# Performance work log

Hardware: AMD Instinct MI355X
Metric: run time of the kernel (lower is better)

## Reference

```python
import jax, jax.numpy as jnp
import numpy as np

B, S, H, E, TOP_K = 4, 2048, 1024, 16, 4


def setup_inputs() -> dict:
    key = jax.random.key(0)
    ks = jax.random.split(key, 12)
    sc = 1.0 / np.sqrt(H)
    inp = {
        "x": jax.random.normal(ks[0], (B, S, H), dtype=jnp.float32),
        "image": jax.random.normal(ks[1], (B, S, H), dtype=jnp.float32),
        "text": jax.random.normal(ks[2], (B, S, H), dtype=jnp.float32),
        "audio": jax.random.normal(ks[3], (B, S, H), dtype=jnp.float32),
        # generalized router linear
        "Wg": jax.random.uniform(ks[4], (H, E), jnp.float32, -sc, sc),
        "bg": jax.random.uniform(ks[5], (E,), jnp.float32, -sc, sc),
        # per-modality router linears
        "Wi": jax.random.uniform(ks[6], (H, E), jnp.float32, -sc, sc),
        "bi": jax.random.uniform(ks[7], (E,), jnp.float32, -sc, sc),
        "Wt": jax.random.uniform(ks[8], (H, E), jnp.float32, -sc, sc),
        "bt": jax.random.uniform(ks[9], (E,), jnp.float32, -sc, sc),
        "Wa": jax.random.uniform(ks[10], (H, E), jnp.float32, -sc, sc),
        "ba": jax.random.uniform(ks[11], (E,), jnp.float32, -sc, sc),
    }
    return inp


def reference(x, image, text, audio, Wg, bg, Wi, bi, Wt, bt, Wa, ba):
    # combined_logits = generalized_router(x) + sum_m modality_router_m(modality_m)
    logits = (
        jnp.einsum("bsh,he->bse", x, Wg) + bg
        + jnp.einsum("bsh,he->bse", image, Wi) + bi
        + jnp.einsum("bsh,he->bse", text, Wt) + bt
        + jnp.einsum("bsh,he->bse", audio, Wa) + ba
    )  # [B,S,E]
    router_probs = jax.nn.softmax(logits, axis=-1)
    top_k_probs, top_k_indices = jax.lax.top_k(router_probs, TOP_K)
    top_k_probs = top_k_probs / jnp.sum(top_k_probs, axis=-1, keepdims=True)
    prob_per_expert = jnp.mean(router_probs, axis=(0, 1))  # [E]
    aux_loss = jnp.sum(prob_per_expert * jnp.log(prob_per_expert * E + 1e-9))
    return (top_k_indices, top_k_probs, aux_loss)
```

## Files before the change

### kernel.cpp

```cpp
#include <hip/hip_runtime.h>
#include <math.h>

constexpr int kTokens = 8192;
constexpr int kH      = 1024;
constexpr int kE      = 16;
constexpr int kTopK   = 4;

template<int NC>
__global__ __launch_bounds__(256, 4)
void router_fmac(const float* __restrict__ x,   const float* __restrict__ img,
                 const float* __restrict__ txt, const float* __restrict__ aud,
                 const float* __restrict__ Wg,  const float* __restrict__ Wi,
                 const float* __restrict__ Wt,  const float* __restrict__ Wa,
                 float* __restrict__ partials)
{
    constexpr int KEXT = 4096 / NC;
    constexpr int P    = KEXT / 16;
    constexpr int MS   = NC / 4;

    __shared__ float xt[2][256 * 20];

    const int t   = threadIdx.x;
    const int w   = t >> 6;
    const int ln  = t & 63;
    const int tq  = ln >> 2;
    const int eq  = ln & 3;
    const int bid = blockIdx.x;
    const int ks  = bid & (NC - 1);
    const int tg  = bid / NC;
    const int m   = ks / MS;
    const int h0  = (ks % MS) * KEXT;
    const int tok0 = tg * 256;

    const float* Xm = (m == 0) ? x  : (m == 1) ? img : (m == 2) ? txt : aud;
    const float* Wm = (m == 0) ? Wg : (m == 1) ? Wi  : (m == 2) ? Wt  : Wa;

    const int sc = t & 3;
    const int sr = t >> 2;
    const float* gbase = Xm + (size_t)tok0 * kH + h0 + sc * 4;

    float4 pf[4];

#pragma unroll
    for (int i = 0; i < 4; ++i)
        pf[i] = *(const float4*)(gbase + (size_t)(sr + 64 * i) * kH);
#pragma unroll
    for (int i = 0; i < 4; ++i)
        *(float4*)&xt[0][(sr + 64 * i) * 20 + sc * 4] = pf[i];
    __syncthreads();

    float facc[4][4];
#pragma unroll
    for (int i = 0; i < 4; ++i)
#pragma unroll
        for (int q = 0; q < 4; ++q) facc[i][q] = 0.f;

    const int r0 = w * 64 + tq;

#pragma unroll
    for (int p = 0; p < P; ++p) {
        if (p < P - 1) {
#pragma unroll
            for (int i = 0; i < 4; ++i)
                pf[i] = *(const float4*)(gbase + (size_t)(sr + 64 * i) * kH + (p + 1) * 16);
        }

        const float* buf = xt[p & 1];
        const float* wp  = Wm + (size_t)(h0 + p * 16) * kE + eq * 4;

#pragma unroll
        for (int hg = 0; hg < 4; ++hg) {
            float4 wv[4];
#pragma unroll
            for (int j = 0; j < 4; ++j)
                wv[j] = *(const float4*)(wp + (hg * 4 + j) * kE);
            float4 xv[4];
#pragma unroll
            for (int i = 0; i < 4; ++i)
                xv[i] = *(const float4*)&buf[(r0 + 16 * i) * 20 + hg * 4];
#pragma unroll
            for (int j = 0; j < 4; ++j) {
#pragma unroll
                for (int i = 0; i < 4; ++i) {
                    const float xh = (j == 0) ? xv[i].x : (j == 1) ? xv[i].y
                                   : (j == 2) ? xv[i].z : xv[i].w;
                    facc[i][0] += xh * wv[j].x;  facc[i][1] += xh * wv[j].y;
                    facc[i][2] += xh * wv[j].z;  facc[i][3] += xh * wv[j].w;
                }
            }
        }

        if (p < P - 1) {
#pragma unroll
            for (int i = 0; i < 4; ++i)
                *(float4*)&xt[(p + 1) & 1][(sr + 64 * i) * 20 + sc * 4] = pf[i];
        }
        __syncthreads();
    }

#pragma unroll
    for (int i = 0; i < 4; ++i) {
        const int token = tok0 + w * 64 + tq + 16 * i;
        *(float4*)&partials[((size_t)ks * kTokens + token) * kE + eq * 4] =
            make_float4(facc[i][0], facc[i][1], facc[i][2], facc[i][3]);
    }
}

template<int NC>
__global__ __launch_bounds__(256)
void router_topk(const float* __restrict__ partials,
                 const float* __restrict__ bg, const float* __restrict__ bi,
                 const float* __restrict__ bt, const float* __restrict__ ba,
                 float* __restrict__ out, float* __restrict__ blocksum)
{
    __shared__ double lgs[64][kE + 1];
    __shared__ float  pr[64][kE + 1];

    const int t    = threadIdx.x;
    const int tq   = t >> 2;
    const int eq   = t & 3;
    const int tok0 = blockIdx.x * 64;

    double a0 = (double)bg[eq*4+0] + (double)bi[eq*4+0] + (double)bt[eq*4+0] + (double)ba[eq*4+0];
    double a1 = (double)bg[eq*4+1] + (double)bi[eq*4+1] + (double)bt[eq*4+1] + (double)ba[eq*4+1];
    double a2 = (double)bg[eq*4+2] + (double)bi[eq*4+2] + (double)bt[eq*4+2] + (double)ba[eq*4+2];
    double a3 = (double)bg[eq*4+3] + (double)bi[eq*4+3] + (double)bt[eq*4+3] + (double)ba[eq*4+3];

#pragma unroll
    for (int c = 0; c < NC; ++c) {
        const float4 v = *(const float4*)(partials + ((size_t)c * kTokens + tok0 + tq) * kE + eq * 4);
        a0 += (double)v.x;  a1 += (double)v.y;  a2 += (double)v.z;  a3 += (double)v.w;
    }
    lgs[tq][eq*4+0] = a0;  lgs[tq][eq*4+1] = a1;
    lgs[tq][eq*4+2] = a2;  lgs[tq][eq*4+3] = a3;
    __syncthreads();

    if (t < 64) {
        const int tok = tok0 + t;
        double lg[kE];
#pragma unroll
        for (int e = 0; e < kE; ++e) lg[e] = lgs[t][e];

        double mx = lg[0];
#pragma unroll
        for (int e = 1; e < kE; ++e) mx = fmax(mx, lg[e]);

        float p[kE];
        float sum = 0.f;
#pragma unroll
        for (int e = 0; e < kE; ++e) {
            p[e] = expf((float)(lg[e] - mx));
            sum += p[e];
        }
        const float inv = 1.f / sum;
#pragma unroll
        for (int e = 0; e < kE; ++e) { p[e] *= inv; pr[t][e] = p[e]; }

        unsigned used = 0;
        float tp[kTopK];
        int   ti[kTopK];
        float s4 = 0.f;
#pragma unroll
        for (int k = 0; k < kTopK; ++k) {
            float best = -1.f;
            int   bidx = 0;
#pragma unroll
            for (int e = 0; e < kE; ++e) {
                if (!((used >> e) & 1u) && p[e] > best) { best = p[e]; bidx = e; }
            }
            used |= 1u << bidx;
            tp[k] = best;
            ti[k] = bidx;
            s4 += best;
        }
        const float rn = 1.f / s4;

        *(float4*)&out[(size_t)tok * kTopK] =
            make_float4((float)ti[0], (float)ti[1], (float)ti[2], (float)ti[3]);
        *(float4*)&out[(size_t)kTokens * kTopK + (size_t)tok * kTopK] =
            make_float4(tp[0] * rn, tp[1] * rn, tp[2] * rn, tp[3] * rn);
    }
    __syncthreads();

    if (t < kE) {
        float s = 0.f;
#pragma unroll
        for (int tk = 0; tk < 64; ++tk) s += pr[tk][t];
        blocksum[blockIdx.x * kE + t] = s;
    }
}

__global__ __launch_bounds__(64)
void router_aux(const float* __restrict__ blocksum, float* __restrict__ out)
{
    __shared__ double ps[kE];
    const int t = threadIdx.x;
    if (t < kE) {
        double s = 0.0;
        for (int b = 0; b < 128; ++b) s += (double)blocksum[b * kE + t];
        ps[t] = s / (double)kTokens;
    }
    __syncthreads();
    if (t == 0) {
        double aux = 0.0;
#pragma unroll
        for (int e = 0; e < kE; ++e) aux += ps[e] * log(ps[e] * (double)kE + 1e-9);
        out[(size_t)kTokens * kTopK * 2] = (float)aux;
    }
}

extern "C" void kernel_launch(void* const* d_in, const int* in_sizes, int n_in,
                              void* d_out, int out_size, void* d_ws, size_t ws_size,
                              hipStream_t stream)
{
    const float* x   = (const float*)d_in[0];
    const float* img = (const float*)d_in[1];
    const float* txt = (const float*)d_in[2];
    const float* aud = (const float*)d_in[3];
    const float* Wg  = (const float*)d_in[4];
    const float* bg  = (const float*)d_in[5];
    const float* Wi  = (const float*)d_in[6];
    const float* bi  = (const float*)d_in[7];
    const float* Wt  = (const float*)d_in[8];
    const float* bt  = (const float*)d_in[9];
    const float* Wa  = (const float*)d_in[10];
    const float* ba  = (const float*)d_in[11];

    float* out = (float*)d_out;

    const size_t need32 = (size_t)32 * kTokens * kE * 4 + 128 * kE * 4;
    if (ws_size >= need32) {
        float* partials = (float*)d_ws;
        float* blocksum = (float*)((char*)d_ws + (size_t)32 * kTokens * kE * 4);
        router_fmac<32><<<1024, 256, 0, stream>>>(x, img, txt, aud, Wg, Wi, Wt, Wa, partials);
        router_topk<32><<<128, 256, 0, stream>>>(partials, bg, bi, bt, ba, out, blocksum);
        router_aux<<<1, 64, 0, stream>>>(blocksum, out);
    } else {
        float* partials = (float*)d_ws;
        float* blocksum = (float*)((char*)d_ws + (size_t)16 * kTokens * kE * 4);
        router_fmac<16><<<512, 256, 0, stream>>>(x, img, txt, aud, Wg, Wi, Wt, Wa, partials);
        router_topk<16><<<128, 256, 0, stream>>>(partials, bg, bi, bt, ba, out, blocksum);
        router_aux<<<1, 64, 0, stream>>>(blocksum, out);
    }
}
```

Before: 211.7 us.

## Drop LDS staging in router matmul; use single-wave blocks with lane-split H and shuffle reduce

The router GEMV kernel no longer stages X tiles through double-buffered shared memory with block barriers. Each 64-lane block now covers 64 tokens, and each lane reads float4 slices of H directly from global memory while computing all 16 experts. A two-step xor-shuffle then reduces across the 4 lanes that share a token. This removes the LDS traffic and __syncthreads, but raises register pressure (64 accumulators per lane) and gives strided, less coalesced global loads.

```diff
diff --git a/kernel.cpp b/kernel.cpp
--- a/kernel.cpp
+++ b/kernel.cpp
@@ -7,7 +7,7 @@
 constexpr int kTopK   = 4;
 
 template<int NC>
-__global__ __launch_bounds__(256, 4)
+__global__ __launch_bounds__(64, 4)
 void router_fmac(const float* __restrict__ x,   const float* __restrict__ img,
                  const float* __restrict__ txt, const float* __restrict__ aud,
                  const float* __restrict__ Wg,  const float* __restrict__ Wi,
@@ -15,94 +15,83 @@
                  float* __restrict__ partials)
 {
     constexpr int KEXT = 4096 / NC;
-    constexpr int P    = KEXT / 16;
+    constexpr int NQ   = KEXT / 16;
     constexpr int MS   = NC / 4;
 
-    __shared__ float xt[2][256 * 20];
-
-    const int t   = threadIdx.x;
-    const int w   = t >> 6;
-    const int ln  = t & 63;
-    const int tq  = ln >> 2;
-    const int eq  = ln & 3;
-    const int bid = blockIdx.x;
-    const int ks  = bid & (NC - 1);
-    const int tg  = bid / NC;
-    const int m   = ks / MS;
-    const int h0  = (ks % MS) * KEXT;
-    const int tok0 = tg * 256;
+    const int ln = threadIdx.x;
+    const int tq = ln >> 2;
+    const int eq = ln & 3;
+    const int ks = blockIdx.x >> 7;
+    const int tg = blockIdx.x & 127;
+    const int m  = ks / MS;
+    const int h0 = (ks % MS) * KEXT;
+    const int tok0 = tg * 64;
 
     const float* Xm = (m == 0) ? x  : (m == 1) ? img : (m == 2) ? txt : aud;
     const float* Wm = (m == 0) ? Wg : (m == 1) ? Wi  : (m == 2) ? Wt  : Wa;
 
-    const int sc = t & 3;
-    const int sr = t >> 2;
-    const float* gbase = Xm + (size_t)tok0 * kH + h0 + sc * 4;
-
-    float4 pf[4];
-
+    float facc[4][kE];
 #pragma unroll
     for (int i = 0; i < 4; ++i)
-        pf[i] = *(const float4*)(gbase + (size_t)(sr + 64 * i) * kH);
+#pragma unroll
+        for (int e = 0; e < kE; ++e) facc[i][e] = 0.f;
+
+    const float* xp[4];
 #pragma unroll
     for (int i = 0; i < 4; ++i)
-        *(float4*)&xt[0][(sr + 64 * i) * 20 + sc * 4] = pf[i];
-    __syncthreads();
-
-    float facc[4][4];
+        xp[i] = Xm + (size_t)(tok0 + tq + 16 * i) * kH + h0 + eq * 4;
+    const float* wp = Wm + (size_t)(h0 + eq * 4) * kE;
+
+#pragma unroll 2
+    for (int q = 0; q < NQ; ++q) {
+        float4 xv[4];
+#pragma unroll
+        for (int i = 0; i < 4; ++i)
+            xv[i] = *(const float4*)(xp[i] + q * 16);
+
+#pragma unroll
+        for (int j = 0; j < 4; ++j) {
+            const float* wr = wp + (size_t)(q * 16 + j) * kE;
+            const float4 w0 = ((const float4*)wr)[0];
+            const float4 w1 = ((const float4*)wr)[1];
+            const float4 w2 = ((const float4*)wr)[2];
+            const float4 w3 = ((const float4*)wr)[3];
+#pragma unroll
+            for (int i = 0; i < 4; ++i) {
+                const float xh = (j == 0) ? xv[i].x : (j == 1) ? xv[i].y
+                               : (j == 2) ? xv[i].z : xv[i].w;
+                facc[i][0]  += xh * w0.x;  facc[i][1]  += xh * w0.y;
+                facc[i][2]  += xh * w0.z;  facc[i][3]  += xh * w0.w;
+                facc[i][4]  += xh * w1.x;  facc[i][5]  += xh * w1.y;
+                facc[i][6]  += xh * w1.z;  facc[i][7]  += xh * w1.w;
+                facc[i][8]  += xh * w2.x;  facc[i][9]  += xh * w2.y;
+                facc[i][10] += xh * w2.z;  facc[i][11] += xh * w2.w;
+                facc[i][12] += xh * w3.x;  facc[i][13] += xh * w3.y;
+                facc[i][14] += xh * w3.z;  facc[i][15] += xh * w3.w;
+            }
+        }
+    }
+
 #pragma unroll
     for (int i = 0; i < 4; ++i)
 #pragma unroll
-        for (int q = 0; q < 4; ++q) facc[i][q] = 0.f;
-
-    const int r0 = w * 64 + tq;
-
-#pragma unroll
-    for (int p = 0; p < P; ++p) {
-        if (p < P - 1) {
-#pragma unroll
-            for (int i = 0; i < 4; ++i)
-                pf[i] = *(const float4*)(gbase + (size_t)(sr + 64 * i) * kH + (p + 1) * 16);
-        }
-
-        const float* buf = xt[p & 1];
-        const float* wp  = Wm + (size_t)(h0 + p * 16) * kE + eq * 4;
-
-#pragma unroll
-        for (int hg = 0; hg < 4; ++hg) {
-            float4 wv[4];
-#pragma unroll
-            for (int j = 0; j < 4; ++j)
-                wv[j] = *(const float4*)(wp + (hg * 4 + j) * kE);
-            float4 xv[4];
-#pragma unroll
-            for (int i = 0; i < 4; ++i)
-                xv[i] = *(const float4*)&buf[(r0 + 16 * i) * 20 + hg * 4];
-#pragma unroll
-            for (int j = 0; j < 4; ++j) {
-#pragma unroll
-                for (int i = 0; i < 4; ++i) {
-                    const float xh = (j == 0) ? xv[i].x : (j == 1) ? xv[i].y
-                                   : (j == 2) ? xv[i].z : xv[i].w;
-                    facc[i][0] += xh * wv[j].x;  facc[i][1] += xh * wv[j].y;
-                    facc[i][2] += xh * wv[j].z;  facc[i][3] += xh * wv[j].w;
-                }
-            }
-        }
-
-        if (p < P - 1) {
-#pragma unroll
-            for (int i = 0; i < 4; ++i)
-                *(float4*)&xt[(p + 1) & 1][(sr + 64 * i) * 20 + sc * 4] = pf[i];
-        }
-        __syncthreads();
-    }
+        for (int e = 0; e < kE; ++e) {
+            float v = facc[i][e];
+            v += __shfl_xor(v, 1, 64);
+            v += __shfl_xor(v, 2, 64);
+            facc[i][e] = v;
+        }
 
 #pragma unroll
     for (int i = 0; i < 4; ++i) {
-        const int token = tok0 + w * 64 + tq + 16 * i;
+        float o0, o1, o2, o3;
+        if (eq == 0)      { o0 = facc[i][0];  o1 = facc[i][1];  o2 = facc[i][2];  o3 = facc[i][3];  }
+        else if (eq == 1) { o0 = facc[i][4];  o1 = facc[i][5];  o2 = facc[i][6];  o3 = facc[i][7];  }
+        else if (eq == 2) { o0 = facc[i][8];  o1 = facc[i][9];  o2 = facc[i][10]; o3 = facc[i][11]; }
+        else              { o0 = facc[i][12]; o1 = facc[i][13]; o2 = facc[i][14]; o3 = facc[i][15]; }
+        const int token = tok0 + tq + 16 * i;
         *(float4*)&partials[((size_t)ks * kTokens + token) * kE + eq * 4] =
-            make_float4(facc[i][0], facc[i][1], facc[i][2], facc[i][3]);
+            make_float4(o0, o1, o2, o3);
     }
 }
 
@@ -232,13 +221,13 @@
     if (ws_size >= need32) {
         float* partials = (float*)d_ws;
         float* blocksum = (float*)((char*)d_ws + (size_t)32 * kTokens * kE * 4);
-        router_fmac<32><<<1024, 256, 0, stream>>>(x, img, txt, aud, Wg, Wi, Wt, Wa, partials);
+        router_fmac<32><<<32 * 128, 64, 0, stream>>>(x, img, txt, aud, Wg, Wi, Wt, Wa, partials);
         router_topk<32><<<128, 256, 0, stream>>>(partials, bg, bi, bt, ba, out, blocksum);
         router_aux<<<1, 64, 0, stream>>>(blocksum, out);
     } else {
         float* partials = (float*)d_ws;
         float* blocksum = (float*)((char*)d_ws + (size_t)16 * kTokens * kE * 4);
-        router_fmac<16><<<512, 256, 0, stream>>>(x, img, txt, aud, Wg, Wi, Wt, Wa, partials);
+        router_fmac<16><<<16 * 128, 64, 0, stream>>>(x, img, txt, aud, Wg, Wi, Wt, Wa, partials);
         router_topk<16><<<128, 256, 0, stream>>>(partials, bg, bi, bt, ba, out, blocksum);
         router_aux<<<1, 64, 0, stream>>>(blocksum, out);
     }
```

After: 229.4 us. 8.3% more time.
